# Kernel optimization log

Measured on AMD Instinct MI355X. Metric: run time of the kernel, lower is better.

The kernel has to match this reference:

```python
import jax, jax.numpy as jnp
import numpy as np

B, A, C = 128, 8732, 21
ALPHA = 1.0
NEG_POS_RATIO = 3


def setup_inputs() -> dict:
    key = jax.random.key(0)
    k1, k2, k3, k4, k5 = jax.random.split(key, 5)
    confidences = jax.random.normal(k1, (B, A, C), dtype=jnp.float32)
    locations = jax.random.normal(k2, (B, A, 4), dtype=jnp.float32)
    gt_locations = jax.random.normal(k3, (B, A, 4), dtype=jnp.float32)
    raw_cls = jax.random.randint(k4, (B, A), 1, C)
    is_pos = jax.random.uniform(k5, (B, A)) < 0.03
    gt_labels = jnp.where(is_pos, raw_cls, 0).astype(jnp.int32)
    return {
        "confidences": confidences,
        "locations": locations,
        "gt_labels": gt_labels,
        "gt_locations": gt_locations,
    }


def reference(confidences, locations, gt_labels, gt_locations):
    pos_mask = gt_labels > 0                     # (B, A)
    neg_avail = gt_labels == 0                   # (B, A)

    # smooth L1 (beta=1) summed over positive anchors
    d = locations - gt_locations                 # (B, A, 4)
    ad = jnp.abs(d)
    sl1 = jnp.where(ad < 1.0, 0.5 * d * d, ad - 0.5)
    loc_loss = jnp.sum(sl1 * pos_mask[..., None].astype(sl1.dtype))

    # per-anchor cross entropy
    logp = jax.nn.log_softmax(confidences, axis=-1)              # (B, A, C)
    ce = -jnp.take_along_axis(logp, gt_labels[..., None].astype(jnp.int32), axis=-1)[..., 0]  # (B, A)

    # hard negative mining: top-(3*num_pos) CE among negatives, per row
    num_pos = jnp.sum(pos_mask, axis=1)                          # (B,)
    num_neg = jnp.minimum(NEG_POS_RATIO * num_pos, jnp.sum(neg_avail, axis=1))
    ce_neg = jnp.where(pos_mask, 0.0, ce)                        # zero out positives (CE >= 0)
    order = jnp.argsort(-ce_neg, axis=1)                         # descending
    ranks = jnp.argsort(order, axis=1)                           # rank of each anchor in descending order
    neg_mask = ranks < num_neg[:, None]

    keep = pos_mask | neg_mask
    conf_loss = jnp.sum(jnp.where(keep, ce, 0.0))

    total_loss = (loc_loss + ALPHA * conf_loss) / jnp.sum(num_pos).astype(loc_loss.dtype)
    return total_loss
```

## Files before the change

### kernel.cpp

```cpp
#include <hip/hip_runtime.h>
#include <math.h>

#define B_ 128
#define A_ 8732
#define C_ 21
#define APB 256
#define NBLK ((A_ + APB - 1) / APB)
#define NPART (B_ * NBLK)

#define OFF_PLOC 0
#define OFF_PPCE 17920
#define OFF_PNP  35840
#define OFF_RCN  53760
#define OFF_RNP  54272
#define OFF_CEN  57344

__global__ __launch_bounds__(256) void k_ce(
        const float* __restrict__ conf, const float* __restrict__ loc,
        const int* __restrict__ lab, const float* __restrict__ gloc,
        float* __restrict__ ce_neg, float* __restrict__ part_loc,
        float* __restrict__ part_pce, int* __restrict__ part_np)
{
    __shared__ float sConf[APB * C_];
    const int b   = blockIdx.y;
    const int a0  = blockIdx.x * APB;
    const int n   = min(APB, A_ - a0);
    const int tid = threadIdx.x;

    {
        const size_t base = ((size_t)b * A_ + a0) * C_;
        const int total = n * C_;
        const int n4 = total >> 2;
        const float4* src4 = (const float4*)(conf + base);
        float4* dst4 = (float4*)sConf;
        for (int i = tid; i < n4; i += 256) dst4[i] = src4[i];
        for (int i = (n4 << 2) + tid; i < total; i += 256) sConf[i] = conf[base + i];
    }
    __syncthreads();

    float pce = 0.f, lloss = 0.f;
    int pcnt = 0;
    if (tid < n) {
        const int a = a0 + tid;
        float v[C_];
        #pragma unroll
        for (int j = 0; j < C_; j++) v[j] = sConf[tid * C_ + j];
        float m = v[0];
        #pragma unroll
        for (int j = 1; j < C_; j++) m = fmaxf(m, v[j]);
        float s = 0.f;
        #pragma unroll
        for (int j = 0; j < C_; j++) s += __expf(v[j] - m);
        const int L = lab[(size_t)b * A_ + a];
        const float ce = __logf(s) + m - v[L];
        const bool pos = (L > 0);
        ce_neg[(size_t)b * A_ + a] = pos ? 0.f : ce;
        if (pos) {
            pce = ce;
            pcnt = 1;
            const float4 lv = ((const float4*)loc)[(size_t)b * A_ + a];
            const float4 gv = ((const float4*)gloc)[(size_t)b * A_ + a];
            float dx = lv.x - gv.x, dy = lv.y - gv.y, dz = lv.z - gv.z, dw = lv.w - gv.w;
            float ax = fabsf(dx), ay = fabsf(dy), az = fabsf(dz), aw = fabsf(dw);
            lloss  = (ax < 1.f) ? 0.5f * dx * dx : ax - 0.5f;
            lloss += (ay < 1.f) ? 0.5f * dy * dy : ay - 0.5f;
            lloss += (az < 1.f) ? 0.5f * dz * dz : az - 0.5f;
            lloss += (aw < 1.f) ? 0.5f * dw * dw : aw - 0.5f;
        }
    }

    #pragma unroll
    for (int off = 32; off > 0; off >>= 1) {
        pce   += __shfl_down(pce, off);
        lloss += __shfl_down(lloss, off);
        pcnt  += __shfl_down(pcnt, off);
    }
    __shared__ float wf[4], wl[4];
    __shared__ int wc[4];
    const int wave = tid >> 6, lane = tid & 63;
    if (lane == 0) { wf[wave] = pce; wl[wave] = lloss; wc[wave] = pcnt; }
    __syncthreads();
    if (tid == 0) {
        const int bid = b * NBLK + blockIdx.x;
        part_loc[bid] = wl[0] + wl[1] + wl[2] + wl[3];
        part_pce[bid] = wf[0] + wf[1] + wf[2] + wf[3];
        part_np[bid]  = wc[0] + wc[1] + wc[2] + wc[3];
    }
}

__device__ __forceinline__ void blk_sum(unsigned vc, float vs,
                                        unsigned* shc, float* shs,
                                        int wave, int lane,
                                        unsigned* outc, float* outs)
{
    #pragma unroll
    for (int off = 32; off > 0; off >>= 1) {
        vc += __shfl_down(vc, off);
        vs += __shfl_down(vs, off);
    }
    __syncthreads();
    if (lane == 0) { shc[wave] = vc; shs[wave] = vs; }
    __syncthreads();
    unsigned tc = 0; float ts = 0.f;
    #pragma unroll
    for (int w = 0; w < 16; w++) { tc += shc[w]; ts += shs[w]; }
    *outc = tc; *outs = ts;
}

__global__ __launch_bounds__(1024) void k_select(
        const float* __restrict__ ce_neg, const int* __restrict__ part_np,
        float* __restrict__ row_cneg, int* __restrict__ row_np)
{
    const int b = blockIdx.x;
    const int tid = threadIdx.x;
    const int wave = tid >> 6, lane = tid & 63;
    const float* ce = ce_neg + (size_t)b * A_;

    __shared__ unsigned shc[16];
    __shared__ float shs[16];
    __shared__ int s_np;

    if (wave == 0) {
        int v = (lane < NBLK) ? part_np[b * NBLK + lane] : 0;
        #pragma unroll
        for (int off = 32; off > 0; off >>= 1) v += __shfl_down(v, off);
        if (lane == 0) s_np = v;
    }

    unsigned keys[9];
    #pragma unroll
    for (int j = 0; j < 9; j++) {
        const int i = tid + j * 1024;
        keys[j] = (i < A_) ? __float_as_uint(ce[i]) : 0u;
    }
    __syncthreads();
    const int np = s_np;
    const int k = min(3 * np, A_ - np);

    float result = 0.f;
    if (k > 0) {
        unsigned c0 = 0; float s0 = 0.f;
        #pragma unroll
        for (int j = 0; j < 9; j++)
            if (keys[j] > 0u) { c0++; s0 += __uint_as_float(keys[j]); }
        unsigned cnt0; float sum0;
        blk_sum(c0, s0, shc, shs, wave, lane, &cnt0, &sum0);

        if (cnt0 < (unsigned)k) {
            result = sum0;
        } else {
            unsigned lo = 0u, hi = 0x7F800000u;
            while (hi - lo > 1u) {
                const unsigned mid = lo + ((hi - lo) >> 1);
                unsigned c = 0;
                #pragma unroll
                for (int j = 0; j < 9; j++) c += (keys[j] > mid) ? 1u : 0u;
                unsigned tot; float dummy;
                blk_sum(c, 0.f, shc, shs, wave, lane, &tot, &dummy);
                if (tot >= (unsigned)k) lo = mid; else hi = mid;
            }
            unsigned c = 0; float s = 0.f;
            #pragma unroll
            for (int j = 0; j < 9; j++)
                if (keys[j] > hi) { c++; s += __uint_as_float(keys[j]); }
            unsigned cg; float sg;
            blk_sum(c, s, shc, shs, wave, lane, &cg, &sg);
            result = sg + (float)(k - (int)cg) * __uint_as_float(hi);
        }
    }

    if (tid == 0) { row_cneg[b] = result; row_np[b] = np; }
}

__global__ __launch_bounds__(1024) void k_final(
        const float* __restrict__ part_loc, const float* __restrict__ part_pce,
        const float* __restrict__ row_cneg, const int* __restrict__ row_np,
        float* __restrict__ out)
{
    const int tid = threadIdx.x;
    const int wave = tid >> 6, lane = tid & 63;
    float s = 0.f;
    for (int i = tid; i < NPART; i += 1024) s += part_loc[i] + part_pce[i];
    int n = 0;
    if (tid < B_) { s += row_cneg[tid]; n = row_np[tid]; }
    #pragma unroll
    for (int off = 32; off > 0; off >>= 1) {
        s += __shfl_down(s, off);
        n += __shfl_down(n, off);
    }
    __shared__ float ws_[16];
    __shared__ int wn_[16];
    if (lane == 0) { ws_[wave] = s; wn_[wave] = n; }
    __syncthreads();
    if (tid == 0) {
        float S = 0.f; int N = 0;
        #pragma unroll
        for (int w = 0; w < 16; w++) { S += ws_[w]; N += wn_[w]; }
        out[0] = S / (float)N;
    }
}

extern "C" void kernel_launch(void* const* d_in, const int* in_sizes, int n_in,
                              void* d_out, int out_size, void* d_ws, size_t ws_size,
                              hipStream_t stream) {
    const float* conf = (const float*)d_in[0];
    const float* loc  = (const float*)d_in[1];
    const int*   lab  = (const int*)d_in[2];
    const float* gloc = (const float*)d_in[3];

    char* ws = (char*)d_ws;
    float* part_loc = (float*)(ws + OFF_PLOC);
    float* part_pce = (float*)(ws + OFF_PPCE);
    int*   part_np  = (int*)(ws + OFF_PNP);
    float* row_cneg = (float*)(ws + OFF_RCN);
    int*   row_np   = (int*)(ws + OFF_RNP);
    float* ce_neg   = (float*)(ws + OFF_CEN);

    dim3 g1(NBLK, B_);
    k_ce<<<g1, 256, 0, stream>>>(conf, loc, lab, gloc, ce_neg,
                                 part_loc, part_pce, part_np);
    k_select<<<B_, 1024, 0, stream>>>(ce_neg, part_np, row_cneg, row_np);
    k_final<<<1, 1024, 0, stream>>>(part_loc, part_pce, row_cneg, row_np,
                                    (float*)d_out);
}
```

Baseline: 195.4 us.

## Use 4-way ballot-based radix search with fewer threads in hard-negative select

The per-row top-k threshold search in k_select moves from a 1024-thread block with a binary search over the float bit pattern to a 256-thread block that holds 35 keys per thread. Each round tests three split points at once using wave ballots and popcounts, packs the three counts into one 64-bit shared word, and lets one thread pick the next interval. This roughly halves the number of search rounds and cuts per-round barrier and reduction cost. The initial upper bound is narrowed to 64.0, which assumes per-anchor cross-entropy stays below that value. Separately, the shared-memory staging in k_ce becomes a fixed unrolled float4 copy with no scalar tail, which relies on the chunk sizes being divisible by 4.

Result: slower. 212.3 us (+8.7%).

```diff
diff --git a/kernel.cpp b/kernel.cpp
--- a/kernel.cpp
+++ b/kernel.cpp
@@ -7,6 +7,7 @@
 #define APB 256
 #define NBLK ((A_ + APB - 1) / APB)
 #define NPART (B_ * NBLK)
+#define KPT 35
 
 #define OFF_PLOC 0
 #define OFF_PPCE 17920
@@ -29,12 +30,14 @@
 
     {
         const size_t base = ((size_t)b * A_ + a0) * C_;
-        const int total = n * C_;
-        const int n4 = total >> 2;
+        const int n4 = (n * C_) >> 2;
         const float4* src4 = (const float4*)(conf + base);
         float4* dst4 = (float4*)sConf;
-        for (int i = tid; i < n4; i += 256) dst4[i] = src4[i];
-        for (int i = (n4 << 2) + tid; i < total; i += 256) sConf[i] = conf[base + i];
+        #pragma unroll
+        for (int j = 0; j < 6; j++) {
+            const int i = tid + j * 256;
+            if (i < n4) dst4[i] = src4[i];
+        }
     }
     __syncthreads();
 
@@ -88,26 +91,7 @@
     }
 }
 
-__device__ __forceinline__ void blk_sum(unsigned vc, float vs,
-                                        unsigned* shc, float* shs,
-                                        int wave, int lane,
-                                        unsigned* outc, float* outs)
-{
-    #pragma unroll
-    for (int off = 32; off > 0; off >>= 1) {
-        vc += __shfl_down(vc, off);
-        vs += __shfl_down(vs, off);
-    }
-    __syncthreads();
-    if (lane == 0) { shc[wave] = vc; shs[wave] = vs; }
-    __syncthreads();
-    unsigned tc = 0; float ts = 0.f;
-    #pragma unroll
-    for (int w = 0; w < 16; w++) { tc += shc[w]; ts += shs[w]; }
-    *outc = tc; *outs = ts;
-}
-
-__global__ __launch_bounds__(1024) void k_select(
+__global__ __launch_bounds__(256) void k_select(
         const float* __restrict__ ce_neg, const int* __restrict__ part_np,
         float* __restrict__ row_cneg, int* __restrict__ row_np)
 {
@@ -116,60 +100,102 @@
     const int wave = tid >> 6, lane = tid & 63;
     const float* ce = ce_neg + (size_t)b * A_;
 
-    __shared__ unsigned shc[16];
-    __shared__ float shs[16];
-    __shared__ int s_np;
+    __shared__ unsigned long long shCnt[4];
+    __shared__ float shS[4];
+    __shared__ int shNp, shK, shMode;
+    __shared__ unsigned shLo, shHi;
+
+    unsigned keys[KPT];
+    #pragma unroll
+    for (int j = 0; j < KPT; j++) {
+        const int i = tid + j * 256;
+        keys[j] = (i < A_) ? __float_as_uint(ce[i]) : 0u;
+    }
 
     if (wave == 0) {
         int v = (lane < NBLK) ? part_np[b * NBLK + lane] : 0;
         #pragma unroll
         for (int off = 32; off > 0; off >>= 1) v += __shfl_down(v, off);
-        if (lane == 0) s_np = v;
-    }
-
-    unsigned keys[9];
-    #pragma unroll
-    for (int j = 0; j < 9; j++) {
-        const int i = tid + j * 1024;
-        keys[j] = (i < A_) ? __float_as_uint(ce[i]) : 0u;
-    }
-    __syncthreads();
-    const int np = s_np;
-    const int k = min(3 * np, A_ - np);
-
-    float result = 0.f;
-    if (k > 0) {
+        if (lane == 0) shNp = v;
+    }
+
+    {
         unsigned c0 = 0; float s0 = 0.f;
         #pragma unroll
-        for (int j = 0; j < 9; j++)
-            if (keys[j] > 0u) { c0++; s0 += __uint_as_float(keys[j]); }
-        unsigned cnt0; float sum0;
-        blk_sum(c0, s0, shc, shs, wave, lane, &cnt0, &sum0);
-
-        if (cnt0 < (unsigned)k) {
-            result = sum0;
-        } else {
-            unsigned lo = 0u, hi = 0x7F800000u;
-            while (hi - lo > 1u) {
-                const unsigned mid = lo + ((hi - lo) >> 1);
-                unsigned c = 0;
-                #pragma unroll
-                for (int j = 0; j < 9; j++) c += (keys[j] > mid) ? 1u : 0u;
-                unsigned tot; float dummy;
-                blk_sum(c, 0.f, shc, shs, wave, lane, &tot, &dummy);
-                if (tot >= (unsigned)k) lo = mid; else hi = mid;
-            }
-            unsigned c = 0; float s = 0.f;
-            #pragma unroll
-            for (int j = 0; j < 9; j++)
-                if (keys[j] > hi) { c++; s += __uint_as_float(keys[j]); }
-            unsigned cg; float sg;
-            blk_sum(c, s, shc, shs, wave, lane, &cg, &sg);
-            result = sg + (float)(k - (int)cg) * __uint_as_float(hi);
-        }
-    }
-
-    if (tid == 0) { row_cneg[b] = result; row_np[b] = np; }
+        for (int j = 0; j < KPT; j++)
+            if (keys[j]) { c0++; s0 += __uint_as_float(keys[j]); }
+        #pragma unroll
+        for (int off = 32; off > 0; off >>= 1) {
+            c0 += __shfl_down(c0, off);
+            s0 += __shfl_down(s0, off);
+        }
+        if (lane == 0) { shCnt[wave] = c0; shS[wave] = s0; }
+    }
+    __syncthreads();
+    if (tid == 0) {
+        const int np = shNp;
+        const int k = min(3 * np, A_ - np);
+        const unsigned cnt0 = (unsigned)(shCnt[0] + shCnt[1] + shCnt[2] + shCnt[3]);
+        const float sum0 = shS[0] + shS[1] + shS[2] + shS[3];
+        row_np[b] = np;
+        if (k <= 0)                    { shMode = 2; row_cneg[b] = 0.f; }
+        else if (cnt0 < (unsigned)k)   { shMode = 2; row_cneg[b] = sum0; }
+        else { shMode = 0; shK = k; shLo = 0u; shHi = 0x42800000u; }
+    }
+    __syncthreads();
+    if (shMode == 2) return;
+
+    const int k = shK;
+    unsigned lo = shLo, hi = shHi;
+    while (hi - lo > 1u) {
+        const unsigned w = hi - lo;
+        unsigned m1, m2, m3;
+        if (w >= 4u) { const unsigned q = w >> 2; m1 = lo + q; m2 = lo + 2*q; m3 = lo + 3*q; }
+        else         { m1 = m2 = m3 = lo + (w >> 1); }
+        unsigned c1 = 0, c2 = 0, c3 = 0;
+        #pragma unroll
+        for (int j = 0; j < KPT; j++) {
+            c1 += (unsigned)__popcll(__ballot(keys[j] > m1));
+            c2 += (unsigned)__popcll(__ballot(keys[j] > m2));
+            c3 += (unsigned)__popcll(__ballot(keys[j] > m3));
+        }
+        if (lane == 0)
+            shCnt[wave] = (unsigned long long)c1
+                        | ((unsigned long long)c2 << 16)
+                        | ((unsigned long long)c3 << 32);
+        __syncthreads();
+        if (tid == 0) {
+            const unsigned long long t = shCnt[0] + shCnt[1] + shCnt[2] + shCnt[3];
+            const int C1 = (int)(t & 0xFFFF), C2 = (int)((t >> 16) & 0xFFFF),
+                      C3 = (int)((t >> 32) & 0xFFFF);
+            unsigned nlo, nhi;
+            if      (C3 >= k) { nlo = m3; nhi = hi; }
+            else if (C2 >= k) { nlo = m2; nhi = m3; }
+            else if (C1 >= k) { nlo = m1; nhi = m2; }
+            else              { nlo = lo; nhi = m1; }
+            shLo = nlo; shHi = nhi;
+        }
+        __syncthreads();
+        lo = shLo; hi = shHi;
+    }
+
+    const unsigned kth = hi;
+    unsigned c = 0; float s = 0.f;
+    #pragma unroll
+    for (int j = 0; j < KPT; j++)
+        if (keys[j] > kth) { c++; s += __uint_as_float(keys[j]); }
+    #pragma unroll
+    for (int off = 32; off > 0; off >>= 1) {
+        c += __shfl_down(c, off);
+        s += __shfl_down(s, off);
+    }
+    if (lane == 0) { shCnt[wave] = c; shS[wave] = s; }
+    __syncthreads();
+    if (tid == 0) {
+        const unsigned Cg = (unsigned)(shCnt[0] + shCnt[1] + shCnt[2] + shCnt[3]);
+        const float Sg = shS[0] + shS[1] + shS[2] + shS[3];
+        row_cneg[b] = Sg + (float)(k - (int)Cg) * __uint_as_float(kth);
+    }
 }
 
 __global__ __launch_bounds__(1024) void k_final(
@@ -219,7 +245,7 @@
     dim3 g1(NBLK, B_);
     k_ce<<<g1, 256, 0, stream>>>(conf, loc, lab, gloc, ce_neg,
                                  part_loc, part_pce, part_np);
-    k_select<<<B_, 1024, 0, stream>>>(ce_neg, part_np, row_cneg, row_np);
+    k_select<<<B_, 256, 0, stream>>>(ce_neg, part_np, row_cneg, row_np);
     k_final<<<1, 1024, 0, stream>>>(part_loc, part_pce, row_cneg, row_np,
                                     (float*)d_out);
 }
```
